# Kernel tuning notes

Measured on AMD Instinct MI355X. Metric: run time of the kernel, lower is better.

Reference implementation:

```python
import jax, jax.numpy as jnp
import numpy as np
import math

H = 5120        # hidden_size
NH = 32         # num heads
HD = H // NH    # head_dim = 160
B = 1
S = 2048
TRAIN_SEQLEN = 8192
BASE = 10000.0


def _rotary_cos_sin(seq_len):
    # Eval-mode RotaryEmbedding: seq_len clamped to training_seqlen, NTK alpha + mscale (logN) scaling.
    eff = max(seq_len, TRAIN_SEQLEN)
    scale = eff / TRAIN_SEQLEN
    mscale = 1.0 if scale <= 1.0 else 0.1 * math.log(scale) + 1.0
    ntk_alpha = max(2 ** math.ceil(math.log(eff / 4096, 2) + 1) - 1, 1)
    base = BASE * ntk_alpha ** (HD / (HD - 2))
    inv_freq = 1.0 / base ** (np.arange(0, HD, 2, dtype=np.float64) / HD)
    t = np.arange(eff, dtype=np.float64)
    freqs = np.outer(t, inv_freq)              # [eff, HD/2]
    emb = np.concatenate([freqs, freqs], axis=-1)  # [eff, HD]
    cos = (mscale * np.cos(emb))[:seq_len].astype(np.float32)
    sin = (mscale * np.sin(emb))[:seq_len].astype(np.float32)
    return jnp.asarray(cos), jnp.asarray(sin)


def _rotate_half(x):
    x1, x2 = x[..., : HD // 2], x[..., HD // 2 :]
    return jnp.concatenate([-x2, x1], axis=-1)


def setup_inputs() -> dict:
    key = jax.random.key(0)
    ks = jax.random.split(key, 6)
    hidden_states = jax.random.normal(ks[0], (B, S, H), jnp.float32)
    residual = jax.random.normal(ks[1], (B, S, H), jnp.float32)
    # boolean causal mask, True = masked (matches masked_fill semantics)
    attention_mask = jnp.triu(jnp.ones((S, S), dtype=bool), k=1)[None, None]
    Wq = jax.random.normal(ks[2], (H, H), jnp.float32) * 0.02      # query: Linear(h, h, bias=False)
    Wkv = jax.random.normal(ks[3], (2 * H, H), jnp.float32) * 0.02  # key_value: Linear(h, 2h, bias=False)
    Wd = jax.random.normal(ks[4], (H, H), jnp.float32) * 0.02       # dense: Linear(h, h) with bias
    bd = jnp.zeros((H,), jnp.float32)
    return {
        "hidden_states": hidden_states,
        "residual": residual,
        "attention_mask": attention_mask,
        "Wq": Wq,
        "Wkv": Wkv,
        "Wd": Wd,
        "bd": bd,
    }


def reference(hidden_states, residual, attention_mask, Wq, Wkv, Wd, bd):
    b, s, h = hidden_states.shape
    # QKV projections (torch Linear: y = x @ W.T)
    q = jnp.einsum('bsh,oh->bso', hidden_states, Wq).reshape(b, s, NH, HD)
    kv = jnp.einsum('bsh,oh->bso', hidden_states, Wkv).reshape(b, s, NH, 2 * HD)
    k, v = kv[..., :HD], kv[..., HD:]
    # rotary embedding with logN mscale folded into cos/sin
    cos, sin = _rotary_cos_sin(s)               # [s, HD]
    cos = cos[None, :, None, :]
    sin = sin[None, :, None, :]
    q = q * cos + _rotate_half(q) * sin
    k = k * cos + _rotate_half(k) * sin
    inv_norm = 1.0 / math.sqrt(HD)
    scores = jnp.einsum('bqnd,bknd->bnqk', q, k) * inv_norm   # [b, nh, s, s]
    scores = jnp.where(attention_mask, jnp.finfo(scores.dtype).min, scores)
    probs = jax.nn.softmax(scores, axis=-1)
    # attention_dropout p=0.0 -> identity
    ctx = jnp.einsum('bnqk,bknd->bqnd', probs, v).reshape(b, s, h)
    out = ctx @ Wd.T + bd
    # dropout_add with hidden_dropout=0.0 (eval) -> residual + out
    return residual + out
```

## Files before the change

kernel.cpp:

```cpp
#include <hip/hip_runtime.h>
#include <cmath>

typedef unsigned short u16;
typedef unsigned int   u32;

using bf16x8 = __attribute__((ext_vector_type(8))) short;
using f32x4  = __attribute__((ext_vector_type(4))) float;

#define S_LEN 2048
#define NHEAD 32
#define HDIM  160
#define HID   5120
#define NQKV  15360

__device__ __forceinline__ f32x4 mfma16(bf16x8 a, bf16x8 b, f32x4 c) {
  return __builtin_amdgcn_mfma_f32_16x16x32_bf16(a, b, c, 0, 0, 0);
}

__device__ __forceinline__ u16 f2bf(float f) {
  u32 u = __builtin_bit_cast(u32, f);
  u += 0x7FFFu + ((u >> 16) & 1u);
  return (u16)(u >> 16);
}
__device__ __forceinline__ float bf2f(u16 h) {
  u32 u = ((u32)h) << 16;
  return __builtin_bit_cast(float, u);
}

__device__ __forceinline__ void gload16(const void* g, void* l) {
  __builtin_amdgcn_global_load_lds((const __attribute__((address_space(1))) void*)g,
                                   (__attribute__((address_space(3))) void*)l, 16, 0, 0);
}

__global__ void cvt_bf16_kernel(const float* __restrict__ in, u16* __restrict__ out, int n8) {
  int i = blockIdx.x * 256 + threadIdx.x;
  if (i >= n8) return;
  const float4* p = (const float4*)in + (size_t)i * 2;
  float4 a = p[0], b = p[1];
  uint4 o;
  o.x = (u32)f2bf(a.x) | ((u32)f2bf(a.y) << 16);
  o.y = (u32)f2bf(a.z) | ((u32)f2bf(a.w) << 16);
  o.z = (u32)f2bf(b.x) | ((u32)f2bf(b.y) << 16);
  o.w = (u32)f2bf(b.z) | ((u32)f2bf(b.w) << 16);
  ((uint4*)out)[i] = o;
}

__global__ void rope_table_kernel(float2* __restrict__ tab) {
  __shared__ double invf_s[80];
  int tid = threadIdx.x;
  if (tid < 80) {
    double base = 10000.0 * pow(3.0, 160.0 / 158.0);
    invf_s[tid] = pow(base, -((double)(2 * tid)) / 160.0);
  }
  __syncthreads();
  for (int i = blockIdx.x * 256 + tid; i < S_LEN * 80; i += gridDim.x * 256) {
    int s = i / 80, j = i % 80;
    double ang = fmod((double)s * invf_s[j], 6.283185307179586476925287);
    float a = (float)ang;
    tab[i] = make_float2(cosf(a), sinf(a));
  }
}

__global__ void rope_apply_kernel(const u16* __restrict__ src, const float2* __restrict__ tab,
                                  u16* __restrict__ dst, int headStride, int rowStride) {
  int i = blockIdx.x * 256 + threadIdx.x;
  if (i >= S_LEN * NHEAD * 80) return;
  int dp = i % 80; int sh = i / 80; int h = sh % NHEAD; int s = sh / NHEAD;
  int d = 2 * dp;
  const u16* row = src + (size_t)s * rowStride + h * headStride;
  u32 q01 = *(const u32*)&row[d];
  u32 p01 = *(const u32*)&row[d < 80 ? d + 80 : d - 80];
  int j = (d < 80) ? d : d - 80;
  float2 cs0 = tab[s * 80 + j];
  float2 cs1 = tab[s * 80 + j + 1];
  float q0 = bf2f((u16)(q01 & 0xffff)), q1 = bf2f((u16)(q01 >> 16));
  float p0 = bf2f((u16)(p01 & 0xffff)), p1 = bf2f((u16)(p01 >> 16));
  float sgn = (d < 80) ? -1.f : 1.f;
  float o0 = q0 * cs0.x + sgn * p0 * cs0.y;
  float o1 = q1 * cs1.x + sgn * p1 * cs1.y;
  u32 o = (u32)f2bf(o0) | ((u32)f2bf(o1) << 16);
  *(u32*)&dst[((size_t)h * S_LEN + s) * HDIM + d] = o;
}

__global__ void vtrans_kernel(const u16* __restrict__ src, u16* __restrict__ Vt, int rowStride) {
  __shared__ u16 T[HDIM][72];
  int h = blockIdx.y; int s0 = blockIdx.x * 64; int tid = threadIdx.x;
  for (int i = tid; i < 64 * 80; i += 256) {
    int s = i / 80, dp = i % 80;
    u32 v = *(const u32*)&src[(size_t)(s0 + s) * rowStride + h * 320 + 2 * dp];
    T[2 * dp][s]     = (u16)(v & 0xffff);
    T[2 * dp + 1][s] = (u16)(v >> 16);
  }
  __syncthreads();
  for (int i = tid; i < HDIM * 32; i += 256) {
    int d = i / 32, sp = i % 32;
    u32 v = (u32)T[d][2 * sp] | ((u32)T[d][2 * sp + 1] << 16);
    *(u32*)&Vt[((size_t)h * HDIM + d) * S_LEN + s0 + 2 * sp] = v;
  }
}

template<int EPI>
__global__ __launch_bounds__(512, 2) void gemm256(
    const u16* __restrict__ A, const u16* __restrict__ Bm, void* __restrict__ Cout,
    int M, int N, int K, const float* __restrict__ bias, const float* __restrict__ resid)
{
  __shared__ u16 As[2][2][8192];
  __shared__ u16 Bs[2][2][8192];
  int tid = threadIdx.x;
  int w = tid >> 6, l = tid & 63, l15 = l & 15, l4 = l >> 4;
  int wr = w >> 2, wc = w & 3;

  int nbx = gridDim.x;
  int nwg = nbx * gridDim.y;
  int lin = blockIdx.y * nbx + blockIdx.x;
  int cpx = nwg >> 3;
  int swz = (lin & 7) * cpx + (lin >> 3);
  int bm = (swz / nbx) * 256, bn = (swz % nbx) * 256;

  int srow = tid >> 2;
  int scol = ((tid & 3) * 8) ^ ((srow & 8) ? 16 : 0);
  const u16* gAr = A  + (size_t)(bm + srow) * K + scol;
  const u16* gBr = Bm + (size_t)(bn + srow) * K + scol;
  int w512 = w * 512;

  f32x4 acc[8][4];
#pragma unroll
  for (int i = 0; i < 8; i++)
#pragma unroll
    for (int j = 0; j < 4; j++) acc[i][j] = f32x4{0.f, 0.f, 0.f, 0.f};

  int cA = (l4 * 8) ^ ((l15 & 8) ? 16 : 0);
  const int NT = K >> 6;
  int arow = wr * 128;
  int brow = (wc >> 1) * 128 + (wc & 1) * 64;

  auto STA = [&](int kt, int kk) { int p = kt & 1, ko = (kt << 6) + (kk << 5);
    gload16(gAr + ko, &As[p][kk][w512]);
    gload16(gAr + (size_t)128 * K + ko, &As[p][kk][4096 + w512]); };
  auto STB = [&](int kt, int kk) { int p = kt & 1, ko = (kt << 6) + (kk << 5);
    gload16(gBr + ko, &Bs[p][kk][w512]);
    gload16(gBr + (size_t)128 * K + ko, &Bs[p][kk][4096 + w512]); };

  STB(0, 0); STA(0, 0); STB(0, 1); STA(0, 1);
  if (NT > 1) { STB(1, 0); STA(1, 0); STB(1, 1); }
  asm volatile("s_waitcnt vmcnt(6)" ::: "memory");
  __builtin_amdgcn_s_barrier();

  for (int kt = 0; kt < NT; ++kt) {
    int p = kt & 1;
    bf16x8 aF[4], bF0[4], bF1[4];

    if (kt + 1 < NT) STA(kt + 1, 1);
#pragma unroll
    for (int mi = 0; mi < 4; ++mi)
      aF[mi] = *(const bf16x8*)&As[p][0][(arow + mi * 16 + l15) * 32 + cA];
#pragma unroll
    for (int ni = 0; ni < 4; ++ni)
      bF0[ni] = *(const bf16x8*)&Bs[p][0][(brow + ni * 16 + l15) * 32 + cA];
    __builtin_amdgcn_s_barrier();
    __builtin_amdgcn_s_setprio(1);
#pragma unroll
    for (int mi = 0; mi < 4; ++mi)
#pragma unroll
      for (int ni = 0; ni < 4; ++ni)
        acc[mi][ni] = mfma16(aF[mi], bF0[ni], acc[mi][ni]);
    __builtin_amdgcn_s_setprio(0);
    __builtin_amdgcn_s_barrier();

    if (kt + 2 < NT) STB(kt + 2, 0);
#pragma unroll
    for (int mi = 0; mi < 4; ++mi)
      aF[mi] = *(const bf16x8*)&As[p][0][(arow + 64 + mi * 16 + l15) * 32 + cA];
    __builtin_amdgcn_s_barrier();
    __builtin_amdgcn_s_setprio(1);
#pragma unroll
    for (int mi = 0; mi < 4; ++mi)
#pragma unroll
      for (int ni = 0; ni < 4; ++ni)
        acc[4 + mi][ni] = mfma16(aF[mi], bF0[ni], acc[4 + mi][ni]);
    __builtin_amdgcn_s_setprio(0);
    __builtin_amdgcn_s_barrier();

    if (kt + 2 < NT) STA(kt + 2, 0);
#pragma unroll
    for (int mi = 0; mi < 4; ++mi)
      aF[mi] = *(const bf16x8*)&As[p][1][(arow + mi * 16 + l15) * 32 + cA];
#pragma unroll
    for (int ni = 0; ni < 4; ++ni)
      bF1[ni] = *(const bf16x8*)&Bs[p][1][(brow + ni * 16 + l15) * 32 + cA];
    __builtin_amdgcn_s_barrier();
    __builtin_amdgcn_s_setprio(1);
#pragma unroll
    for (int mi = 0; mi < 4; ++mi)
#pragma unroll
      for (int ni = 0; ni < 4; ++ni)
        acc[mi][ni] = mfma16(aF[mi], bF1[ni], acc[mi][ni]);
    __builtin_amdgcn_s_setprio(0);
    __builtin_amdgcn_s_barrier();

    if (kt + 2 < NT) STB(kt + 2, 1);
#pragma unroll
    for (int mi = 0; mi < 4; ++mi)
      aF[mi] = *(const bf16x8*)&As[p][1][(arow + 64 + mi * 16 + l15) * 32 + cA];
    __builtin_amdgcn_s_barrier();
    __builtin_amdgcn_s_setprio(1);
#pragma unroll
    for (int mi = 0; mi < 4; ++mi)
#pragma unroll
      for (int ni = 0; ni < 4; ++ni)
        acc[4 + mi][ni] = mfma16(aF[mi], bF1[ni], acc[4 + mi][ni]);
    __builtin_amdgcn_s_setprio(0);
    if (kt + 2 < NT)      asm volatile("s_waitcnt vmcnt(6)" ::: "memory");
    else if (kt + 1 < NT) asm volatile("s_waitcnt vmcnt(0)" ::: "memory");
    __builtin_amdgcn_s_barrier();
  }

#pragma unroll
  for (int mi = 0; mi < 8; ++mi)
#pragma unroll
    for (int ni = 0; ni < 4; ++ni) {
      int row0 = bm + wr * 128 + mi * 16 + l4 * 4;
      int col  = bn + wc * 64 + ni * 16 + l15;
      if (EPI == 0) {
        u16* C = (u16*)Cout;
#pragma unroll
        for (int r = 0; r < 4; r++) C[(size_t)(row0 + r) * N + col] = f2bf(acc[mi][ni][r]);
      } else {
        float* C = (float*)Cout;
        float b = bias[col];
#pragma unroll
        for (int r = 0; r < 4; r++) {
          size_t idx = (size_t)(row0 + r) * N + col;
          C[idx] = acc[mi][ni][r] + b + resid[idx];
        }
      }
    }
}

template<int EPI>
__global__ __launch_bounds__(256, 2) void gemm_bt(
    const u16* __restrict__ A, const u16* __restrict__ Bm, void* __restrict__ Cout,
    int M, int N, int K, const float* __restrict__ bias, const float* __restrict__ resid)
{
  int tid = threadIdx.x;
  int wv = tid >> 6, l = tid & 63, l15 = l & 15, l4 = l >> 4;
  int nbx = gridDim.x;
  int nwg = nbx * gridDim.y;
  int lin = blockIdx.y * nbx + blockIdx.x;
  int cpx = nwg >> 3;
  int swz = (lin & 7) * cpx + (lin >> 3);
  int bm = (swz / nbx) * 128, bn = (swz % nbx) * 128;

  __shared__ u16 As[128 * 32], Bs[128 * 32];
  f32x4 acc[4][4];
#pragma unroll
  for (int i = 0; i < 4; i++)
#pragma unroll
    for (int j = 0; j < 4; j++) acc[i][j] = f32x4{0.f, 0.f, 0.f, 0.f};

  int wm = (wv >> 1) * 64, wn = (wv & 1) * 64;
  const u16* gA = A + (size_t)(bm + (tid >> 2)) * K + (tid & 3) * 8;
  const u16* gB = Bm + (size_t)(bn + (tid >> 2)) * K + (tid & 3) * 8;
  u16* ldsA = As + wv * 16 * 32;
  u16* ldsB = Bs + wv * 16 * 32;

  for (int k0 = 0; k0 < K; k0 += 32) {
    __syncthreads();
    gload16(gA + k0, ldsA);
    gload16(gA + (size_t)64 * K + k0, ldsA + 64 * 32);
    gload16(gB + k0, ldsB);
    gload16(gB + (size_t)64 * K + k0, ldsB + 64 * 32);
    __syncthreads();
    bf16x8 af[4], bfr[4];
#pragma unroll
    for (int i = 0; i < 4; i++) af[i] = *(const bf16x8*)&As[(wm + i * 16 + l15) * 32 + l4 * 8];
#pragma unroll
    for (int i = 0; i < 4; i++) bfr[i] = *(const bf16x8*)&Bs[(wn + i * 16 + l15) * 32 + l4 * 8];
#pragma unroll
    for (int mi = 0; mi < 4; mi++)
#pragma unroll
      for (int ni = 0; ni < 4; ni++) acc[mi][ni] = mfma16(af[mi], bfr[ni], acc[mi][ni]);
  }

#pragma unroll
  for (int mi = 0; mi < 4; mi++)
#pragma unroll
    for (int ni = 0; ni < 4; ni++) {
      int row0 = bm + wm + mi * 16 + l4 * 4;
      int col  = bn + wn + ni * 16 + l15;
      if (EPI == 0) {
        u16* C = (u16*)Cout;
#pragma unroll
        for (int r = 0; r < 4; r++) C[(size_t)(row0 + r) * N + col] = f2bf(acc[mi][ni][r]);
      } else {
        float* C = (float*)Cout;
        float b = bias[col];
#pragma unroll
        for (int r = 0; r < 4; r++) {
          size_t idx = (size_t)(row0 + r) * N + col;
          C[idx] = acc[mi][ni][r] + b + resid[idx];
        }
      }
    }
}

__global__ __launch_bounds__(512, 4) void attn_kernel(
    const u16* __restrict__ Qr, const u16* __restrict__ Kr,
    const u16* __restrict__ Vt, u16* __restrict__ ctx)
{
  int lin = blockIdx.x;
  int h  = lin & 31;
  int qx = (lin < 256) ? (15 - (lin >> 5)) : ((lin - 256) >> 5);
  int q0 = qx * 128;
  int tid = threadIdx.x;
  int w = tid >> 6, l = tid & 63, l15 = l & 15, l4 = l >> 4;
  int qb = q0 + w * 16;

  __shared__ u16 Ks[64][164];
  __shared__ u16 Vs[160][68];
  __shared__ u16 Plds[8][16][68];

  const u16* Qh = Qr + (size_t)h * S_LEN * HDIM;
  const u16* Kh = Kr + (size_t)h * S_LEN * HDIM;
  const u16* Vh = Vt + (size_t)h * HDIM * S_LEN;

  bf16x8 aQ[5];
#pragma unroll
  for (int kc = 0; kc < 5; kc++)
    aQ[kc] = *(const bf16x8*)&Qh[(size_t)(qb + l15) * HDIM + kc * 32 + l4 * 8];

  f32x4 accO[10];
#pragma unroll
  for (int dt = 0; dt < 10; dt++) accO[dt] = f32x4{0.f, 0.f, 0.f, 0.f};
  float mrun[4], lrun[4];
#pragma unroll
  for (int r = 0; r < 4; r++) { mrun[r] = -1e30f; lrun[r] = 0.f; }

  const float c2 = 0.07905694150420949f * 1.44269504088896f;
  int Tend = 2 * qx + 2;

  {
    uint4 rg[5];
#pragma unroll
    for (int i = 0; i < 5; i++) {
      int u = tid + 512 * i;
      if (u < 1280) { int row = u / 20, c = u % 20;
        rg[i] = *(const uint4*)&Kh[(size_t)row * HDIM + c * 8]; }
      else { int v = u - 1280; int row = v >> 3, c = v & 7;
        rg[i] = *(const uint4*)&Vh[(size_t)row * S_LEN + c * 8]; }
    }
#pragma unroll
    for (int i = 0; i < 5; i++) {
      int u = tid + 512 * i;
      if (u < 1280) { int row = u / 20, c = u % 20; *(uint4*)&Ks[row][c * 8] = rg[i]; }
      else { int v = u - 1280; int row = v >> 3, c = v & 7; *(uint4*)&Vs[row][c * 8] = rg[i]; }
    }
  }
  __syncthreads();

  for (int t = 0; t < Tend; ++t) {
    int k0 = t * 64;
    bool more = (t + 1 < Tend);
    uint4 rg[5];
    if (more) {
      int k1 = k0 + 64;
#pragma unroll
      for (int i = 0; i < 5; i++) {
        int u = tid + 512 * i;
        if (u < 1280) { int row = u / 20, c = u % 20;
          rg[i] = *(const uint4*)&Kh[(size_t)(k1 + row) * HDIM + c * 8]; }
        else { int v = u - 1280; int row = v >> 3, c = v & 7;
          rg[i] = *(const uint4*)&Vh[(size_t)row * S_LEN + k1 + c * 8]; }
      }
    }

    if (k0 <= qb + 15) {
      f32x4 s_[4];
#pragma unroll
      for (int nt = 0; nt < 4; nt++) s_[nt] = f32x4{0.f, 0.f, 0.f, 0.f};

#pragma unroll
      for (int kc = 0; kc < 5; kc++) {
        bf16x8 bK[4];
#pragma unroll
        for (int nt = 0; nt < 4; nt++)
          bK[nt] = *(const bf16x8*)&Ks[nt * 16 + l15][kc * 32 + l4 * 8];
        __builtin_amdgcn_s_setprio(1);
#pragma unroll
        for (int nt = 0; nt < 4; nt++) s_[nt] = mfma16(aQ[kc], bK[nt], s_[nt]);
        __builtin_amdgcn_s_setprio(0);
      }

      if (k0 + 63 > qb) {
#pragma unroll
        for (int nt = 0; nt < 4; nt++)
#pragma unroll
          for (int r = 0; r < 4; r++) {
            int kk = k0 + nt * 16 + l15;
            int qq = qb + l4 * 4 + r;
            if (kk > qq) s_[nt][r] = -1e30f;
          }
      }

      float sf[4];
#pragma unroll
      for (int r = 0; r < 4; r++) {
        float v = fmaxf(fmaxf(s_[0][r], s_[1][r]), fmaxf(s_[2][r], s_[3][r]));
#pragma unroll
        for (int m = 1; m <= 8; m <<= 1) v = fmaxf(v, __shfl_xor(v, m));
        float mnew = fmaxf(mrun[r], v);
        sf[r] = exp2f((mrun[r] - mnew) * c2);
        mrun[r] = mnew;
      }
      float rsum[4] = {0.f, 0.f, 0.f, 0.f};
#pragma unroll
      for (int nt = 0; nt < 4; nt++)
#pragma unroll
        for (int r = 0; r < 4; r++) {
          float p = exp2f((s_[nt][r] - mrun[r]) * c2);
          s_[nt][r] = p;
          rsum[r] += p;
        }
#pragma unroll
      for (int r = 0; r < 4; r++) {
        float v = rsum[r];
#pragma unroll
        for (int m = 1; m <= 8; m <<= 1) v += __shfl_xor(v, m);
        lrun[r] = lrun[r] * sf[r] + v;
      }
#pragma unroll
      for (int dt = 0; dt < 10; dt++)
#pragma unroll
        for (int r = 0; r < 4; r++) accO[dt][r] *= sf[r];
#pragma unroll
      for (int nt = 0; nt < 4; nt++)
#pragma unroll
        for (int r = 0; r < 4; r++)
          Plds[w][l4 * 4 + r][nt * 16 + l15] = f2bf(s_[nt][r]);

#pragma unroll
      for (int kc = 0; kc < 2; kc++) {
        bf16x8 aP = *(const bf16x8*)&Plds[w][l15][kc * 32 + l4 * 8];
        bf16x8 bV[10];
#pragma unroll
        for (int dt = 0; dt < 10; dt++)
          bV[dt] = *(const bf16x8*)&Vs[dt * 16 + l15][kc * 32 + l4 * 8];
        __builtin_amdgcn_s_setprio(1);
#pragma unroll
        for (int dt = 0; dt < 10; dt++)
          accO[dt] = mfma16(aP, bV[dt], accO[dt]);
        __builtin_amdgcn_s_setprio(0);
      }
    }

    __builtin_amdgcn_s_barrier();
    if (more) {
#pragma unroll
      for (int i = 0; i < 5; i++) {
        int u = tid + 512 * i;
        if (u < 1280) { int row = u / 20, c = u % 20; *(uint4*)&Ks[row][c * 8] = rg[i]; }
        else { int v = u - 1280; int row = v >> 3, c = v & 7; *(uint4*)&Vs[row][c * 8] = rg[i]; }
      }
      asm volatile("s_waitcnt lgkmcnt(0)" ::: "memory");
    }
    __builtin_amdgcn_s_barrier();
  }

  float inv[4];
#pragma unroll
  for (int r = 0; r < 4; r++) inv[r] = 1.0f / lrun[r];
#pragma unroll
  for (int dt = 0; dt < 10; dt++)
#pragma unroll
    for (int r = 0; r < 4; r++) {
      int q = qb + l4 * 4 + r;
      ctx[(size_t)q * HID + h * HDIM + dt * 16 + l15] = f2bf(accO[dt][r] * inv[r]);
    }
}

extern "C" void kernel_launch(void* const* d_in, const int* in_sizes, int n_in,
                              void* d_out, int out_size, void* d_ws, size_t ws_size,
                              hipStream_t stream) {
  const float* hs    = (const float*)d_in[0];
  const float* resid = (const float*)d_in[1];
  const float* Wq  = (const float*)d_in[3];
  const float* Wkv = (const float*)d_in[4];
  const float* Wd  = (const float*)d_in[5];
  const float* bd  = (const float*)d_in[6];
  float* out = (float*)d_out;

  char* ws = (char*)d_ws;
  const size_t SH = (size_t)S_LEN * HID;
  u16* Xb     = (u16*)(ws);                        size_t off = SH * 2;
  u16* Wqkvb  = (u16*)(ws + off);                  off += (size_t)3 * HID * HID * 2;
  u16* Wdb    = (u16*)(ws + off);                  off += (size_t)HID * HID * 2;
  u16* QKVraw = (u16*)(ws + off);                  off += (size_t)S_LEN * NQKV * 2;
  u16* Qr     = (u16*)(ws + off);                  off += SH * 2;
  u16* Kr     = (u16*)(ws + off);                  off += SH * 2;
  u16* Vt     = (u16*)(ws + off);                  off += SH * 2;
  u16* ctx    = (u16*)(ws + off);                  off += SH * 2;
  float2* tab = (float2*)(ws + off);               off += (size_t)S_LEN * 80 * 8;

  cvt_bf16_kernel<<<(int)(SH / 8 / 256), 256, 0, stream>>>(hs, Xb, (int)(SH / 8));
  cvt_bf16_kernel<<<HID * HID / 8 / 256, 256, 0, stream>>>(Wq, Wqkvb, HID * HID / 8);
  cvt_bf16_kernel<<<2 * HID * HID / 8 / 256, 256, 0, stream>>>(Wkv, Wqkvb + (size_t)HID * HID, 2 * HID * HID / 8);
  cvt_bf16_kernel<<<HID * HID / 8 / 256, 256, 0, stream>>>(Wd, Wdb, HID * HID / 8);

  rope_table_kernel<<<64, 256, 0, stream>>>(tab);

  gemm256<0><<<dim3(NQKV / 256, S_LEN / 256), 512, 0, stream>>>(
      Xb, Wqkvb, QKVraw, S_LEN, NQKV, HID, nullptr, nullptr);

  rope_apply_kernel<<<S_LEN * NHEAD * 80 / 256, 256, 0, stream>>>(QKVraw, tab, Qr, HDIM, NQKV);
  rope_apply_kernel<<<S_LEN * NHEAD * 80 / 256, 256, 0, stream>>>(QKVraw + HID, tab, Kr, 2 * HDIM, NQKV);
  vtrans_kernel<<<dim3(S_LEN / 64, NHEAD), 256, 0, stream>>>(QKVraw + HID + HDIM, Vt, NQKV);

  attn_kernel<<<512, 512, 0, stream>>>(Qr, Kr, Vt, ctx);

  gemm_bt<1><<<dim3(HID / 128, S_LEN / 128), 256, 0, stream>>>(
      ctx, Wdb, out, S_LEN, HID, HID, bd, resid);
}
```

Before: 980.8 us.

## Fuse fp32 weight-to-bf16 conversion into the QKV and output-projection GEMM loads

Drops the three separate weight conversion kernels and the bf16 weight buffers. Both GEMMs now read fp32 weights straight from global memory into registers, convert them to bf16 and store them to LDS, with the B-tile pipeline and waitcnts reworked to match. This removes a full read-and-write pass over roughly 100M weight elements. In exchange, each GEMM block re-reads fp32 weights (twice the bytes, repeated across row blocks), and the B path loses the direct global-to-LDS loads, which could slow the main GEMM loop.

```diff
diff --git a/kernel.cpp b/kernel.cpp
--- a/kernel.cpp
+++ b/kernel.cpp
@@ -25,6 +25,14 @@
 __device__ __forceinline__ float bf2f(u16 h) {
   u32 u = ((u32)h) << 16;
   return __builtin_bit_cast(float, u);
+}
+__device__ __forceinline__ bf16x8 cvt8(float4 a, float4 b) {
+  bf16x8 r;
+  r[0] = (short)f2bf(a.x); r[1] = (short)f2bf(a.y);
+  r[2] = (short)f2bf(a.z); r[3] = (short)f2bf(a.w);
+  r[4] = (short)f2bf(b.x); r[5] = (short)f2bf(b.y);
+  r[6] = (short)f2bf(b.z); r[7] = (short)f2bf(b.w);
+  return r;
 }
 
 __device__ __forceinline__ void gload16(const void* g, void* l) {
@@ -99,10 +107,9 @@
   }
 }
 
-template<int EPI>
-__global__ __launch_bounds__(512, 2) void gemm256(
-    const u16* __restrict__ A, const u16* __restrict__ Bm, void* __restrict__ Cout,
-    int M, int N, int K, const float* __restrict__ bias, const float* __restrict__ resid)
+__global__ __launch_bounds__(512, 2) void gemm256_qkv(
+    const u16* __restrict__ A, const float* __restrict__ Bq, const float* __restrict__ Bkv,
+    u16* __restrict__ Cout, int M, int N, int K)
 {
   __shared__ u16 As[2][2][8192];
   __shared__ u16 Bs[2][2][8192];
@@ -119,8 +126,10 @@
 
   int srow = tid >> 2;
   int scol = ((tid & 3) * 8) ^ ((srow & 8) ? 16 : 0);
-  const u16* gAr = A  + (size_t)(bm + srow) * K + scol;
-  const u16* gBr = Bm + (size_t)(bn + srow) * K + scol;
+  const u16* gAr = A + (size_t)(bm + srow) * K + scol;
+  const float* Bsrc = (bn < HID) ? Bq + (size_t)bn * K : Bkv + (size_t)(bn - HID) * K;
+  const float* gBa = Bsrc + (size_t)srow * K + scol;
+  const float* gBb = gBa + (size_t)128 * K;
   int w512 = w * 512;
 
   f32x4 acc[8][4];
@@ -137,18 +146,32 @@
   auto STA = [&](int kt, int kk) { int p = kt & 1, ko = (kt << 6) + (kk << 5);
     gload16(gAr + ko, &As[p][kk][w512]);
     gload16(gAr + (size_t)128 * K + ko, &As[p][kk][4096 + w512]); };
-  auto STB = [&](int kt, int kk) { int p = kt & 1, ko = (kt << 6) + (kk << 5);
-    gload16(gBr + ko, &Bs[p][kk][w512]);
-    gload16(gBr + (size_t)128 * K + ko, &Bs[p][kk][4096 + w512]); };
-
-  STB(0, 0); STA(0, 0); STB(0, 1); STA(0, 1);
-  if (NT > 1) { STB(1, 0); STA(1, 0); STB(1, 1); }
+
+  float4 s0, s1, s2, s3;
+#define LDB(kt, kk) { int ko = ((kt) << 6) + ((kk) << 5);                      \
+    s0 = *(const float4*)(gBa + ko); s1 = *(const float4*)(gBa + ko + 4);      \
+    s2 = *(const float4*)(gBb + ko); s3 = *(const float4*)(gBb + ko + 4); }
+#define WRB(pp, kk) {                                                          \
+    *(bf16x8*)&Bs[pp][kk][tid * 8]        = cvt8(s0, s1);                      \
+    *(bf16x8*)&Bs[pp][kk][4096 + tid * 8] = cvt8(s2, s3); }
+
+  LDB(0, 0);
+  asm volatile("s_waitcnt vmcnt(0)" ::: "memory");
+  WRB(0, 0);
+  LDB(0, 1);
+  asm volatile("s_waitcnt vmcnt(0)" ::: "memory");
+  WRB(0, 1);
+  STA(0, 0); STA(0, 1);
+  STA(1, 0);
+  LDB(1, 0);
   asm volatile("s_waitcnt vmcnt(6)" ::: "memory");
+  asm volatile("s_waitcnt lgkmcnt(0)" ::: "memory");
   __builtin_amdgcn_s_barrier();
+
+  bf16x8 aF[4], bF0[4], bF1[4];
 
   for (int kt = 0; kt < NT; ++kt) {
     int p = kt & 1;
-    bf16x8 aF[4], bF0[4], bF1[4];
 
     if (kt + 1 < NT) STA(kt + 1, 1);
 #pragma unroll
@@ -167,10 +190,15 @@
     __builtin_amdgcn_s_setprio(0);
     __builtin_amdgcn_s_barrier();
 
-    if (kt + 2 < NT) STB(kt + 2, 0);
+    if (kt + 1 < NT) {
+      asm volatile("s_waitcnt vmcnt(2)" ::: "memory");
+      WRB(p ^ 1, 0);
+      LDB(kt + 1, 1);
+    }
 #pragma unroll
     for (int mi = 0; mi < 4; ++mi)
       aF[mi] = *(const bf16x8*)&As[p][0][(arow + 64 + mi * 16 + l15) * 32 + cA];
+    asm volatile("s_waitcnt lgkmcnt(0)" ::: "memory");
     __builtin_amdgcn_s_barrier();
     __builtin_amdgcn_s_setprio(1);
 #pragma unroll
@@ -198,10 +226,16 @@
     __builtin_amdgcn_s_setprio(0);
     __builtin_amdgcn_s_barrier();
 
-    if (kt + 2 < NT) STB(kt + 2, 1);
+    if (kt + 1 < NT) {
+      if (kt + 2 < NT) asm volatile("s_waitcnt vmcnt(2)" ::: "memory");
+      else             asm volatile("s_waitcnt vmcnt(0)" ::: "memory");
+      WRB(p ^ 1, 1);
+      if (kt + 2 < NT) LDB(kt + 2, 0);
+    }
 #pragma unroll
     for (int mi = 0; mi < 4; ++mi)
       aF[mi] = *(const bf16x8*)&As[p][1][(arow + 64 + mi * 16 + l15) * 32 + cA];
+    asm volatile("s_waitcnt lgkmcnt(0)" ::: "memory");
     __builtin_amdgcn_s_barrier();
     __builtin_amdgcn_s_setprio(1);
 #pragma unroll
@@ -210,10 +244,10 @@
       for (int ni = 0; ni < 4; ++ni)
         acc[4 + mi][ni] = mfma16(aF[mi], bF1[ni], acc[4 + mi][ni]);
     __builtin_amdgcn_s_setprio(0);
-    if (kt + 2 < NT)      asm volatile("s_waitcnt vmcnt(6)" ::: "memory");
-    else if (kt + 1 < NT) asm volatile("s_waitcnt vmcnt(0)" ::: "memory");
-    __builtin_amdgcn_s_barrier();
-  }
+    __builtin_amdgcn_s_barrier();
+  }
+#undef LDB
+#undef WRB
 
 #pragma unroll
   for (int mi = 0; mi < 8; ++mi)
@@ -221,25 +255,13 @@
     for (int ni = 0; ni < 4; ++ni) {
       int row0 = bm + wr * 128 + mi * 16 + l4 * 4;
       int col  = bn + wc * 64 + ni * 16 + l15;
-      if (EPI == 0) {
-        u16* C = (u16*)Cout;
-#pragma unroll
-        for (int r = 0; r < 4; r++) C[(size_t)(row0 + r) * N + col] = f2bf(acc[mi][ni][r]);
-      } else {
-        float* C = (float*)Cout;
-        float b = bias[col];
-#pragma unroll
-        for (int r = 0; r < 4; r++) {
-          size_t idx = (size_t)(row0 + r) * N + col;
-          C[idx] = acc[mi][ni][r] + b + resid[idx];
-        }
-      }
-    }
-}
-
-template<int EPI>
-__global__ __launch_bounds__(256, 2) void gemm_bt(
-    const u16* __restrict__ A, const u16* __restrict__ Bm, void* __restrict__ Cout,
+#pragma unroll
+      for (int r = 0; r < 4; r++) Cout[(size_t)(row0 + r) * N + col] = f2bf(acc[mi][ni][r]);
+    }
+}
+
+__global__ __launch_bounds__(256, 2) void gemm_proj(
+    const u16* __restrict__ A, const float* __restrict__ Bf, float* __restrict__ Cout,
     int M, int N, int K, const float* __restrict__ bias, const float* __restrict__ resid)
 {
   int tid = threadIdx.x;
@@ -260,17 +282,32 @@
 
   int wm = (wv >> 1) * 64, wn = (wv & 1) * 64;
   const u16* gA = A + (size_t)(bm + (tid >> 2)) * K + (tid & 3) * 8;
-  const u16* gB = Bm + (size_t)(bn + (tid >> 2)) * K + (tid & 3) * 8;
+  const float* gB = Bf + (size_t)(bn + (tid >> 2)) * K + (tid & 3) * 8;
   u16* ldsA = As + wv * 16 * 32;
-  u16* ldsB = Bs + wv * 16 * 32;
+
+  float4 s0, s1, s2, s3;
+  s0 = *(const float4*)(gB);      s1 = *(const float4*)(gB + 4);
+  s2 = *(const float4*)(gB + (size_t)64 * K); s3 = *(const float4*)(gB + (size_t)64 * K + 4);
 
   for (int k0 = 0; k0 < K; k0 += 32) {
-    __syncthreads();
+    __builtin_amdgcn_s_barrier();
     gload16(gA + k0, ldsA);
     gload16(gA + (size_t)64 * K + k0, ldsA + 64 * 32);
-    gload16(gB + k0, ldsB);
-    gload16(gB + (size_t)64 * K + k0, ldsB + 64 * 32);
-    __syncthreads();
+    asm volatile("s_waitcnt vmcnt(2)" ::: "memory");
+    *(bf16x8*)&As[0] = *(bf16x8*)&As[0];
+    *(bf16x8*)&Bs[tid * 8]        = cvt8(s0, s1);
+    *(bf16x8*)&Bs[2048 + tid * 8] = cvt8(s2, s3);
+    bool more = (k0 + 32) < K;
+    if (more) {
+      s0 = *(const float4*)(gB + k0 + 32);      s1 = *(const float4*)(gB + k0 + 36);
+      s2 = *(const float4*)(gB + (size_t)64 * K + k0 + 32);
+      s3 = *(const float4*)(gB + (size_t)64 * K + k0 + 36);
+      asm volatile("s_waitcnt vmcnt(4)" ::: "memory");
+    } else {
+      asm volatile("s_waitcnt vmcnt(0)" ::: "memory");
+    }
+    asm volatile("s_waitcnt lgkmcnt(0)" ::: "memory");
+    __builtin_amdgcn_s_barrier();
     bf16x8 af[4], bfr[4];
 #pragma unroll
     for (int i = 0; i < 4; i++) af[i] = *(const bf16x8*)&As[(wm + i * 16 + l15) * 32 + l4 * 8];
@@ -288,18 +325,11 @@
     for (int ni = 0; ni < 4; ni++) {
       int row0 = bm + wm + mi * 16 + l4 * 4;
       int col  = bn + wn + ni * 16 + l15;
-      if (EPI == 0) {
-        u16* C = (u16*)Cout;
-#pragma unroll
-        for (int r = 0; r < 4; r++) C[(size_t)(row0 + r) * N + col] = f2bf(acc[mi][ni][r]);
-      } else {
-        float* C = (float*)Cout;
-        float b = bias[col];
-#pragma unroll
-        for (int r = 0; r < 4; r++) {
-          size_t idx = (size_t)(row0 + r) * N + col;
-          C[idx] = acc[mi][ni][r] + b + resid[idx];
-        }
+      float b = bias[col];
+#pragma unroll
+      for (int r = 0; r < 4; r++) {
+        size_t idx = (size_t)(row0 + r) * N + col;
+        Cout[idx] = acc[mi][ni][r] + b + resid[idx];
       }
     }
 }
@@ -492,8 +522,6 @@
   char* ws = (char*)d_ws;
   const size_t SH = (size_t)S_LEN * HID;
   u16* Xb     = (u16*)(ws);                        size_t off = SH * 2;
-  u16* Wqkvb  = (u16*)(ws + off);                  off += (size_t)3 * HID * HID * 2;
-  u16* Wdb    = (u16*)(ws + off);                  off += (size_t)HID * HID * 2;
   u16* QKVraw = (u16*)(ws + off);                  off += (size_t)S_LEN * NQKV * 2;
   u16* Qr     = (u16*)(ws + off);                  off += SH * 2;
   u16* Kr     = (u16*)(ws + off);                  off += SH * 2;
@@ -502,14 +530,11 @@
   float2* tab = (float2*)(ws + off);               off += (size_t)S_LEN * 80 * 8;
 
   cvt_bf16_kernel<<<(int)(SH / 8 / 256), 256, 0, stream>>>(hs, Xb, (int)(SH / 8));
-  cvt_bf16_kernel<<<HID * HID / 8 / 256, 256, 0, stream>>>(Wq, Wqkvb, HID * HID / 8);
-  cvt_bf16_kernel<<<2 * HID * HID / 8 / 256, 256, 0, stream>>>(Wkv, Wqkvb + (size_t)HID * HID, 2 * HID * HID / 8);
-  cvt_bf16_kernel<<<HID * HID / 8 / 256, 256, 0, stream>>>(Wd, Wdb, HID * HID / 8);
 
   rope_table_kernel<<<64, 256, 0, stream>>>(tab);
 
-  gemm256<0><<<dim3(NQKV / 256, S_LEN / 256), 512, 0, stream>>>(
-      Xb, Wqkvb, QKVraw, S_LEN, NQKV, HID, nullptr, nullptr);
+  gemm256_qkv<<<dim3(NQKV / 256, S_LEN / 256), 512, 0, stream>>>(
+      Xb, Wq, Wkv, QKVraw, S_LEN, NQKV, HID);
 
   rope_apply_kernel<<<S_LEN * NHEAD * 80 / 256, 256, 0, stream>>>(QKVraw, tab, Qr, HDIM, NQKV);
   rope_apply_kernel<<<S_LEN * NHEAD * 80 / 256, 256, 0, stream>>>(QKVraw + HID, tab, Kr, 2 * HDIM, NQKV);
@@ -517,6 +542,6 @@
 
   attn_kernel<<<512, 512, 0, stream>>>(Qr, Kr, Vt, ctx);
 
-  gemm_bt<1><<<dim3(HID / 128, S_LEN / 128), 256, 0, stream>>>(
-      ctx, Wdb, out, S_LEN, HID, HID, bd, resid);
-}
+  gemm_proj<<<dim3(HID / 128, S_LEN / 128), 256, 0, stream>>>(
+      ctx, Wd, out, S_LEN, HID, HID, bd, resid);
+}
```

After: 1.060 ms. 8.1% more time.
